# Kernel optimization log

Hardware: AMD Instinct MI355X
Metric: run time of the kernel (lower is better)

## Reference

```python
import jax, jax.numpy as jnp
import numpy as np

EPS = 1e-6


def setup_inputs() -> dict:
    key = jax.random.key(0)
    ks = jax.random.split(key, 7)
    b, n, d, H, hid = 4, 512, 128, 4, 32
    scale1 = 1.0 / np.sqrt(2 * d)
    scale2 = 1.0 / np.sqrt(hid)
    return {
        "x": jax.random.normal(ks[0], (b, n, d), dtype=jnp.float32),
        "W1": jax.random.normal(ks[1], (H, 2 * d, hid), dtype=jnp.float32) * scale1,
        "b1": jax.random.normal(ks[2], (H, hid), dtype=jnp.float32) * scale1,
        "W2": jax.random.normal(ks[3], (H, hid), dtype=jnp.float32) * scale2,
        "b2": jax.random.normal(ks[4], (H,), dtype=jnp.float32) * scale2,
        "Wp": jax.random.normal(ks[5], (d, d), dtype=jnp.float32) / np.sqrt(d),
        "bp": jax.random.normal(ks[6], (d,), dtype=jnp.float32) / np.sqrt(d),
    }


def reference(x, W1, b1, W2, b2, Wp, bp):
    # x: [b, n, d]; W1: [H, 2d, hid]; W2: [H, hid]
    d = x.shape[-1]
    # squared pairwise distance via gram matrix: ||xi - xj||^2
    sq = jnp.sum(x * x, axis=-1)                                   # [b, n]
    gram = jnp.einsum("bnd,bmd->bnm", x, x)                        # [b, n, n]
    dist2 = jnp.maximum(sq[:, :, None] + sq[:, None, :] - 2.0 * gram, 0.0)
    # per-head first linear on cat([xi, xj]) split into two projections
    ai = jnp.einsum("bnd,hdk->bhnk", x, W1[:, :d, :])              # [b, H, n, hid]
    aj = jnp.einsum("bnd,hdk->bhnk", x, W1[:, d:, :])              # [b, H, n, hid]
    pre = jnp.tanh(ai[:, :, :, None, :] + aj[:, :, None, :, :]
                   + b1[None, :, None, None, :])                   # [b, H, n, n, hid]
    sigma = jax.nn.softplus(jnp.einsum("bhnmk,hk->bhnm", pre, W2)
                            + b2[None, :, None, None])             # [b, H, n, n]
    adj = jnp.exp(-dist2[:, None, :, :] / (2.0 * sigma * sigma + EPS))
    adj_mean = jnp.mean(adj, axis=1)                               # [b, n, n]
    h = jnp.einsum("bnm,bmd->bnd", adj_mean, x)                    # [b, n, d]
    return h @ Wp + bp
```

## Files before the change

kernel.cpp:

```cpp
#include <hip/hip_runtime.h>

typedef float v4f __attribute__((ext_vector_type(4)));
typedef float v2f __attribute__((ext_vector_type(2)));

#define LOG2E   1.4426950408889634f
#define NLOG2E (-1.4426950408889634f)
#define C2L2E   2.8853900817779268f
#define NM2L2E (-2.8853900817779268f)
#define LN2     0.6931471805599453f

__device__ __forceinline__ float fexp2(float x){ return __builtin_amdgcn_exp2f(x); }
__device__ __forceinline__ float flog2(float x){ return __builtin_amdgcn_logf(x); }
__device__ __forceinline__ float frcp (float x){ return __builtin_amdgcn_rcpf(x); }
__device__ __forceinline__ float hsum(v4f v){ return (v.x+v.y)+(v.z+v.w); }

__global__ __launch_bounds__(256) void prep_kernel(
    const float* __restrict__ x, const float* __restrict__ W1,
    const float* __restrict__ b1, const float* __restrict__ Wp,
    float* __restrict__ sq, float* __restrict__ Abuf,
    float* __restrict__ Bbuf, float* __restrict__ xpT)
{
  const int bid = blockIdx.x, t = threadIdx.x;
  if (bid >= 192) {
    int row = (bid - 192) * 256 + t;
    const v4f* xv = (const v4f*)(x + row * 128);
    float s = 0.f;
#pragma unroll
    for (int q = 0; q < 32; q++) { v4f v = xv[q]; s += hsum(v * v); }
    sq[row] = s;
    return;
  }
  __shared__ v4f Xs[64 * 9];
  __shared__ v4f Ws[32 * 16];
  const bool isAB = bid < 128;
  int it, ct;
  if (isAB) { it = bid >> 2; ct = bid & 3; }
  else      { int q = bid - 128; it = q >> 1; ct = q & 1; }
  const int row0 = it * 64;
  const int tx = t & 15, ty = t >> 4;
  const int r0 = ty * 4, c0 = tx * 4;
  v4f acc[4] = {};

  for (int dd0 = 0; dd0 < 128; dd0 += 32) {
    __syncthreads();
#pragma unroll
    for (int s2 = 0; s2 < 2; s2++) {
      int idx = t + s2 * 256;
      int row = idx >> 3, k4 = idx & 7;
      v4f v = *(const v4f*)(x + (row0 + row) * 128 + dd0 + k4 * 4);
      Xs[row * 9 + ((k4 + (row >> 2)) & 7)] = v;
    }
#pragma unroll
    for (int s2 = 0; s2 < 2; s2++) {
      int idx = t + s2 * 256;
      int dd = idx >> 4, cf4 = idx & 15;
      v4f v;
      if (isAB) {
        int cl = cf4 * 4; int half = cl >> 5; int k = cl & 31;
        v = *(const v4f*)(W1 + (ct * 256 + half * 128 + dd0 + dd) * 32 + k);
      } else {
        v = *(const v4f*)(Wp + (dd0 + dd) * 128 + ct * 64 + cf4 * 4);
      }
      Ws[dd * 16 + cf4] = v;
    }
    __syncthreads();
#pragma unroll
    for (int dd4 = 0; dd4 < 8; dd4++) {
      int sa = (dd4 + ty) & 7;
      v4f a0 = Xs[(r0 + 0) * 9 + sa], a1 = Xs[(r0 + 1) * 9 + sa];
      v4f a2 = Xs[(r0 + 2) * 9 + sa], a3 = Xs[(r0 + 3) * 9 + sa];
#pragma unroll
      for (int u = 0; u < 4; u++) {
        v4f bv = Ws[(dd4 * 4 + u) * 16 + tx];
        acc[0] += a0[u] * bv; acc[1] += a1[u] * bv;
        acc[2] += a2[u] * bv; acc[3] += a3[u] * bv;
      }
    }
  }

  if (isAB) {
    const int h = ct; const int half = c0 >> 5; const int k = c0 & 31;
    v4f bias = {};
    if (half == 0) bias = *(const v4f*)(b1 + h * 32 + k);
    float* dst = (half == 0) ? Abuf : Bbuf;
#pragma unroll
    for (int i = 0; i < 4; i++) {
      int rg = row0 + r0 + i; int b = rg >> 9; int ir = rg & 511;
      v4f o = (acc[i] + bias) * C2L2E;
      v4f eo = { fexp2(o.x), fexp2(o.y), fexp2(o.z), fexp2(o.w) };
      *(v4f*)(dst + ((b * 4 + h) * 512 + ir) * 32 + k) = eo;
    }
  } else {
    int rg0 = row0 + r0; int b = rg0 >> 9; int ir0 = rg0 & 511;
#pragma unroll
    for (int u = 0; u < 4; u++) {
      int c = ct * 64 + c0 + u;
      v4f o = { acc[0][u], acc[1][u], acc[2][u], acc[3][u] };
      *(v4f*)(xpT + (b * 128 + c) * 512 + ir0) = o;
    }
  }
}

__global__ __launch_bounds__(256) void adj_kernel(
    const float* __restrict__ x, const float* __restrict__ sq,
    const float* __restrict__ Abuf, const float* __restrict__ Bbuf,
    const float* __restrict__ W2, const float* __restrict__ b2g,
    float* __restrict__ ADJ)
{
  const int jt = blockIdx.x;
  const int it = blockIdx.y;
  const int b  = blockIdx.z;
  const int t = threadIdx.x, tx = t & 15, ty = t >> 4;
  const int c0 = 2 * tx;
  __shared__ v4f Bs[2 * 32 * 9];
  __shared__ v4f W2s[32];
  __shared__ v2f W2p[32];
  __shared__ float hb[4];

  if (t < 32) {
    v4f w = ((const v4f*)W2)[t] * NM2L2E;
    W2s[t] = w;
    v2f p = { w.x + w.y, w.z + w.w };
    W2p[t] = p;
  }
  if (t < 4) {
    float s = b2g[t];
    for (int k = 0; k < 32; k++) s += W2[t * 32 + k];
    hb[t] = s * LOG2E;
  }

  const int s_col = (t >> 3) & 31, s_k4 = t & 7;
  const int s_slot = (s_k4 + (s_col >> 1) + ((s_col >> 4) << 2)) & 7;

  const int rsh = (tx >> 3) << 2;

  const float* xb = x + (size_t)b * 512 * 128;
  const int irow = it * 16 + ty;
  const float* xi  = xb + irow * 128;
  const float* xjc = xb + (jt * 32) * 128;

  v4f gacc0 = {}, gacc1 = {};
  for (int half = 0; half < 2; half++) {
    if (half) __syncthreads();
#pragma unroll
    for (int s = 0; s < 2; s++) {
      Bs[s * 288 + s_col * 9 + s_slot] =
        *(const v4f*)(xjc + s_col * 128 + half * 64 + s * 32 + s_k4 * 4);
    }
    __syncthreads();
#pragma unroll
    for (int sec = 0; sec < 2; sec++) {
#pragma unroll
      for (int k4 = 0; k4 < 8; k4++) {
        v4f a0 = *(const v4f*)(xi + half * 64 + sec * 32 + k4 * 4);
        int sb = (k4 + tx + rsh) & 7;
        v4f b0  = Bs[sec * 288 + (c0 + 0) * 9 + sb];
        v4f b1v = Bs[sec * 288 + (c0 + 1) * 9 + sb];
        gacc0 += a0 * b0; gacc1 += a0 * b1v;
      }
    }
  }
  float si  = sq[b * 512 + irow];
  float sj0 = sq[b * 512 + jt * 32 + c0], sj1 = sq[b * 512 + jt * 32 + c0 + 1];
  float d2L0 = fmaxf(si + sj0 - 2.f * hsum(gacc0), 0.f) * NLOG2E;
  float d2L1 = fmaxf(si + sj1 - 2.f * hsum(gacc1), 0.f) * NLOG2E;

  float accA0 = 0.f, accA1 = 0.f;
  for (int g = 0; g < 2; g++) {
    __syncthreads();
#pragma unroll
    for (int s = 0; s < 2; s++) {
      Bs[s * 288 + s_col * 9 + s_slot] =
        *(const v4f*)(Bbuf + ((size_t)((b * 4 + g * 2 + s) * 512 + jt * 32 + s_col)) * 32 + s_k4 * 4);
    }
    __syncthreads();
#pragma unroll
    for (int hh = 0; hh < 2; hh++) {
      int h = g * 2 + hh;
      const float* A0 = Abuf + ((size_t)((b * 4 + h) * 512 + irow)) * 32;
      float hbv = hb[h];
      float s0 = hbv, s1 = hbv;
#pragma unroll
      for (int k4 = 0; k4 < 8; k4++) {
        v4f a0 = *(const v4f*)(A0 + k4 * 4);
        int sb = (k4 + tx + rsh) & 7;
        v4f bv0 = Bs[hh * 288 + (c0 + 0) * 9 + sb];
        v4f bv1 = Bs[hh * 288 + (c0 + 1) * 9 + sb];
        v4f w  = W2s[h * 8 + k4];
        v2f wp = W2p[h * 8 + k4];
        {
          v4f e = a0 * bv0;
          float d01 = fmaf(e.x, e.y, e.x + e.y) + 1.f;
          float d23 = fmaf(e.z, e.w, e.z + e.w) + 1.f;
          float n01 = fmaf(w.x, e.y, wp.x); n01 = fmaf(w.y, e.x, n01);
          float n23 = fmaf(w.z, e.w, wp.y); n23 = fmaf(w.w, e.z, n23);
          float num = fmaf(n01, d23, n23 * d01);
          s0 = fmaf(num, frcp(d01 * d23), s0);
        }
        {
          v4f e = a0 * bv1;
          float d01 = fmaf(e.x, e.y, e.x + e.y) + 1.f;
          float d23 = fmaf(e.z, e.w, e.z + e.w) + 1.f;
          float n01 = fmaf(w.x, e.y, wp.x); n01 = fmaf(w.y, e.x, n01);
          float n23 = fmaf(w.z, e.w, wp.y); n23 = fmaf(w.w, e.z, n23);
          float num = fmaf(n01, d23, n23 * d01);
          s1 = fmaf(num, frcp(d01 * d23), s1);
        }
      }
      float u20 = fexp2(s0), u21 = fexp2(s1);
      float sg0 = LN2 * flog2(1.f + u20);
      float sg1 = LN2 * flog2(1.f + u21);
      float den0 = fmaf(2.f * sg0, sg0, 1e-6f);
      float den1 = fmaf(2.f * sg1, sg1, 1e-6f);
      float rr = frcp(den0 * den1);
      accA0 += fexp2(d2L0 * (rr * den1));
      accA1 += fexp2(d2L1 * (rr * den0));
    }
  }
  v2f o = { accA0 * 0.25f, accA1 * 0.25f };
  *(v2f*)(ADJ + ((size_t)(b * 512 + irow)) * 512 + jt * 32 + c0) = o;
}

__global__ __launch_bounds__(256) void out_gemm(
    const float* __restrict__ ADJ, const float* __restrict__ xpT,
    float* __restrict__ part)
{
  const int ct = blockIdx.x;
  const int it = blockIdx.y;
  const int z = blockIdx.z; const int b = z >> 2, ks = z & 3;
  const int t = threadIdx.x, tx = t & 15, ty = t >> 4;
  const int r0 = 2 * ty, c0 = 2 * tx;
  __shared__ v4f Ajs[32 * 9], Xps[32 * 9];
  v4f acc[4] = {};
  const int row = t >> 3, k4l = t & 7, slot = (k4l + (row >> 1)) & 7;

  for (int k0 = ks * 128; k0 < ks * 128 + 128; k0 += 32) {
    __syncthreads();
    Ajs[row * 9 + slot] = *(const v4f*)(ADJ + ((size_t)(b * 512 + it * 32 + row)) * 512 + k0 + k4l * 4);
    Xps[row * 9 + slot] = *(const v4f*)(xpT + ((size_t)(b * 128 + ct * 32 + row)) * 512 + k0 + k4l * 4);
    __syncthreads();
#pragma unroll
    for (int k4 = 0; k4 < 8; k4++) {
      int sa = (k4 + ty) & 7, sb = (k4 + tx) & 7;
      v4f a0 = Ajs[(r0 + 0) * 9 + sa], a1 = Ajs[(r0 + 1) * 9 + sa];
      v4f b0 = Xps[(c0 + 0) * 9 + sb], b1v = Xps[(c0 + 1) * 9 + sb];
      acc[0] += a0 * b0; acc[1] += a0 * b1v;
      acc[2] += a1 * b0; acc[3] += a1 * b1v;
    }
  }
  float* dst = part + ((size_t)((ks * 4 + b) * 512 + it * 32 + r0)) * 128 + ct * 32 + c0;
  v2f o0 = { hsum(acc[0]), hsum(acc[1]) };
  v2f o1 = { hsum(acc[2]), hsum(acc[3]) };
  *(v2f*)dst = o0;
  *(v2f*)(dst + 128) = o1;
}

__global__ __launch_bounds__(256) void reduce_out(
    const float* __restrict__ part, const float* __restrict__ bp,
    float* __restrict__ out)
{
  int g = blockIdx.x * 256 + threadIdx.x;
  const v4f* p = (const v4f*)part;
  v4f s = (p[g] + p[g + 65536]) + (p[g + 131072] + p[g + 196608]);
  v4f bv = ((const v4f*)bp)[g & 31];
  ((v4f*)out)[g] = s + bv;
}

extern "C" void kernel_launch(void* const* d_in, const int* in_sizes, int n_in,
                              void* d_out, int out_size, void* d_ws, size_t ws_size,
                              hipStream_t stream) {
  const float* x  = (const float*)d_in[0];
  const float* W1 = (const float*)d_in[1];
  const float* b1 = (const float*)d_in[2];
  const float* W2 = (const float*)d_in[3];
  const float* b2 = (const float*)d_in[4];
  const float* Wp = (const float*)d_in[5];
  const float* bp = (const float*)d_in[6];
  float* out = (float*)d_out;

  float* ws  = (float*)d_ws;
  float* sq  = ws;
  float* EA  = ws + 2048;
  float* EB  = EA + 262144;
  float* xpT = EB + 262144;
  float* ADJ = xpT + 262144;
  float* part = ADJ + 1048576;

  prep_kernel<<<200, 256, 0, stream>>>(x, W1, b1, Wp, sq, EA, EB, xpT);
  adj_kernel<<<dim3(16, 32, 4), 256, 0, stream>>>(x, sq, EA, EB, W2, b2, ADJ);
  out_gemm<<<dim3(4, 16, 16), 256, 0, stream>>>(ADJ, xpT, part);
  reduce_out<<<256, 256, 0, stream>>>(part, bp, out);
}
```

Baseline: 57.70 us.

## Fuse split-K output GEMM and reduction into one full-K kernel

Replaces the split-K out_gemm plus separate reduce_out pass with a single kernel in which each block covers the full 512-long K dimension and adds the bias directly. Each block stages xpT tiles in shared memory and streams ADJ rows straight from global memory, with 16 rows by 32 columns per block. This removes one kernel launch and the write and reread of the partial-sum buffer. The cost is longer serial K loops per thread, 512 blocks instead of 1024, and unshared global loads of ADJ repeated across the column tiles.

Result: slower. 60.75 us (+5.3%).

```diff
diff --git a/kernel.cpp b/kernel.cpp
--- a/kernel.cpp
+++ b/kernel.cpp
@@ -221,49 +221,48 @@
   *(v2f*)(ADJ + ((size_t)(b * 512 + irow)) * 512 + jt * 32 + c0) = o;
 }
 
-__global__ __launch_bounds__(256) void out_gemm(
+__global__ __launch_bounds__(256) void out_kernel(
     const float* __restrict__ ADJ, const float* __restrict__ xpT,
-    float* __restrict__ part)
+    const float* __restrict__ bp, float* __restrict__ out)
 {
   const int ct = blockIdx.x;
   const int it = blockIdx.y;
-  const int z = blockIdx.z; const int b = z >> 2, ks = z & 3;
+  const int b  = blockIdx.z;
   const int t = threadIdx.x, tx = t & 15, ty = t >> 4;
-  const int r0 = 2 * ty, c0 = 2 * tx;
-  __shared__ v4f Ajs[32 * 9], Xps[32 * 9];
-  v4f acc[4] = {};
-  const int row = t >> 3, k4l = t & 7, slot = (k4l + (row >> 1)) & 7;
-
-  for (int k0 = ks * 128; k0 < ks * 128 + 128; k0 += 32) {
-    __syncthreads();
-    Ajs[row * 9 + slot] = *(const v4f*)(ADJ + ((size_t)(b * 512 + it * 32 + row)) * 512 + k0 + k4l * 4);
-    Xps[row * 9 + slot] = *(const v4f*)(xpT + ((size_t)(b * 128 + ct * 32 + row)) * 512 + k0 + k4l * 4);
-    __syncthreads();
-#pragma unroll
-    for (int k4 = 0; k4 < 8; k4++) {
-      int sa = (k4 + ty) & 7, sb = (k4 + tx) & 7;
-      v4f a0 = Ajs[(r0 + 0) * 9 + sa], a1 = Ajs[(r0 + 1) * 9 + sa];
-      v4f b0 = Xps[(c0 + 0) * 9 + sb], b1v = Xps[(c0 + 1) * 9 + sb];
-      acc[0] += a0 * b0; acc[1] += a0 * b1v;
-      acc[2] += a1 * b0; acc[3] += a1 * b1v;
-    }
-  }
-  float* dst = part + ((size_t)((ks * 4 + b) * 512 + it * 32 + r0)) * 128 + ct * 32 + c0;
-  v2f o0 = { hsum(acc[0]), hsum(acc[1]) };
-  v2f o1 = { hsum(acc[2]), hsum(acc[3]) };
-  *(v2f*)dst = o0;
-  *(v2f*)(dst + 128) = o1;
-}
-
-__global__ __launch_bounds__(256) void reduce_out(
-    const float* __restrict__ part, const float* __restrict__ bp,
-    float* __restrict__ out)
-{
-  int g = blockIdx.x * 256 + threadIdx.x;
-  const v4f* p = (const v4f*)part;
-  v4f s = (p[g] + p[g + 65536]) + (p[g + 131072] + p[g + 196608]);
-  v4f bv = ((const v4f*)bp)[g & 31];
-  ((v4f*)out)[g] = s + bv;
+  const int c0 = 2 * tx;
+  __shared__ v4f Bs[2 * 32 * 9];
+  const int s_col = (t >> 3) & 31, s_k4 = t & 7;
+  const int s_slot = (s_k4 + (s_col >> 1) + ((s_col >> 4) << 2)) & 7;
+  const int rsh = (tx >> 3) << 2;
+
+  const int irow = it * 16 + ty;
+  const float* ai  = ADJ + ((size_t)(b * 512 + irow)) * 512;
+  const float* xjc = xpT + ((size_t)(b * 128 + ct * 32)) * 512;
+
+  v4f acc0 = {}, acc1 = {};
+  for (int j0 = 0; j0 < 512; j0 += 64) {
+    if (j0) __syncthreads();
+#pragma unroll
+    for (int s = 0; s < 2; s++) {
+      Bs[s * 288 + s_col * 9 + s_slot] =
+        *(const v4f*)(xjc + s_col * 512 + j0 + s * 32 + s_k4 * 4);
+    }
+    __syncthreads();
+#pragma unroll
+    for (int sec = 0; sec < 2; sec++) {
+#pragma unroll
+      for (int k4 = 0; k4 < 8; k4++) {
+        v4f a0 = *(const v4f*)(ai + j0 + sec * 32 + k4 * 4);
+        int sb = (k4 + tx + rsh) & 7;
+        v4f b0  = Bs[sec * 288 + (c0 + 0) * 9 + sb];
+        v4f b1v = Bs[sec * 288 + (c0 + 1) * 9 + sb];
+        acc0 += a0 * b0; acc1 += a0 * b1v;
+      }
+    }
+  }
+  int c = ct * 32 + c0;
+  v2f o = { hsum(acc0) + bp[c], hsum(acc1) + bp[c + 1] };
+  *(v2f*)(out + ((size_t)(b * 512 + irow)) * 128 + c) = o;
 }
 
 extern "C" void kernel_launch(void* const* d_in, const int* in_sizes, int n_in,
@@ -284,10 +283,8 @@
   float* EB  = EA + 262144;
   float* xpT = EB + 262144;
   float* ADJ = xpT + 262144;
-  float* part = ADJ + 1048576;
 
   prep_kernel<<<200, 256, 0, stream>>>(x, W1, b1, Wp, sq, EA, EB, xpT);
   adj_kernel<<<dim3(16, 32, 4), 256, 0, stream>>>(x, sq, EA, EB, W2, b2, ADJ);
-  out_gemm<<<dim3(4, 16, 16), 256, 0, stream>>>(ADJ, xpT, part);
-  reduce_out<<<256, 256, 0, stream>>>(part, bp, out);
-}
+  out_kernel<<<dim3(4, 32, 4), 256, 0, stream>>>(ADJ, xpT, bp, out);
+}
```
